# Performance work log

Measured on AMD Instinct MI355X. Metric: run time of the kernel, lower is better.

## Reference

```python
import jax, jax.numpy as jnp
import numpy as np

B, S, H = 1, 2048, 1024
E, F, K = 8, 3584, 2


def setup_inputs() -> dict:
    key = jax.random.key(0)
    ks = jax.random.split(key, 5)
    scale_h = 1.0 / np.sqrt(H)
    scale_f = 1.0 / np.sqrt(F)
    return {
        "hidden_states": jax.random.normal(ks[0], (B, S, H), dtype=jnp.float32),
        "gate_w": jax.random.normal(ks[1], (E, H), dtype=jnp.float32) * scale_h,
        "w1": jax.random.normal(ks[2], (E, F, H), dtype=jnp.float32) * scale_h,
        "w2": jax.random.normal(ks[3], (E, H, F), dtype=jnp.float32) * scale_f,
        "w3": jax.random.normal(ks[4], (E, F, H), dtype=jnp.float32) * scale_h,
    }


def reference(hidden_states, gate_w, w1, w2, w3):
    b, s, h = hidden_states.shape
    x = hidden_states.reshape(-1, h)                      # [T, H]
    T = x.shape[0]
    router_logits = x @ gate_w.T                          # [T, E]
    probs = jax.nn.softmax(router_logits.astype(jnp.float32), axis=-1)
    rw, sel = jax.lax.top_k(probs, K)                     # [T, K]
    rw = rw / jnp.sum(rw, axis=-1, keepdims=True)
    rw = rw.astype(x.dtype)
    # combine weights per (token, expert): scatter top-k routing weights
    combine = jnp.zeros((T, E), dtype=x.dtype).at[
        jnp.arange(T)[:, None], sel
    ].add(rw)                                             # [T, E]
    out = jnp.zeros_like(x)
    for e in range(E):  # small fixed expert count
        # SwiGLU expert FFN (F.linear: x @ W.T)
        hmid = jax.nn.silu(x @ w1[e].T) * (x @ w3[e].T)   # [T, F]
        out = out + combine[:, e:e + 1] * (hmid @ w2[e].T)
    return out.reshape(b, s, h), router_logits
```

## Files before the change

kernel.cpp:

```cpp
#include <hip/hip_runtime.h>
#include <hip/hip_bf16.h>
#include <math.h>

namespace {
constexpr int kT = 2048;
constexpr int kH = 1024;
constexpr int kE = 8;
constexpr int kF = 3584;
constexpr int kK = 2;

constexpr size_t OFF_CNT  = 0;
constexpr size_t OFF_LIST = 1024;
constexpr size_t OFF_RW   = OFF_LIST + sizeof(int) * kE * kT;
constexpr size_t OFF_HMID = 1u << 20;
constexpr size_t OFF_XB   = 32u << 20;
constexpr size_t SZ_XB    = (size_t)kT * kH * 2;
constexpr size_t SZ_W     = (size_t)kE * kF * kH * 2;
constexpr size_t OFF_W1B  = OFF_XB + SZ_XB;
constexpr size_t OFF_W3B  = OFF_W1B + SZ_W;
constexpr size_t OFF_W2B  = OFF_W3B + SZ_W;
constexpr size_t WS_NEED  = OFF_W2B + SZ_W;

constexpr long NX8  = (long)kT * kH / 8;
constexpr long NW8  = (long)kE * kF * kH / 8;
constexpr long TOT8 = NX8 + 3 * NW8;

typedef __attribute__((ext_vector_type(8))) short bf16x8;
typedef __attribute__((ext_vector_type(4))) float fx4;
}

__device__ __forceinline__ short f2bf_s(float f) {
  union { __hip_bfloat16 h; short s; } u;
  u.h = __float2bfloat16(f);
  return u.s;
}

__device__ __forceinline__ bf16x8 pack8(float4 a, float4 b) {
  bf16x8 r;
  r[0] = f2bf_s(a.x); r[1] = f2bf_s(a.y);
  r[2] = f2bf_s(a.z); r[3] = f2bf_s(a.w);
  r[4] = f2bf_s(b.x); r[5] = f2bf_s(b.y);
  r[6] = f2bf_s(b.z); r[7] = f2bf_s(b.w);
  return r;
}

__device__ __forceinline__ bf16x8 pack8v(fx4 a, fx4 b) {
  bf16x8 r;
  r[0] = f2bf_s(a[0]); r[1] = f2bf_s(a[1]);
  r[2] = f2bf_s(a[2]); r[3] = f2bf_s(a[3]);
  r[4] = f2bf_s(b[0]); r[5] = f2bf_s(b[1]);
  r[6] = f2bf_s(b[2]); r[7] = f2bf_s(b[3]);
  return r;
}

__device__ __forceinline__ int swz(int row, int u) {
  return row * 64 + ((u ^ (row & 7)) << 3);
}

__device__ __forceinline__ void gload16(const void* g, void* l) {
  __builtin_amdgcn_global_load_lds(
      (const __attribute__((address_space(1))) void*)g,
      (__attribute__((address_space(3))) void*)l, 16, 0, 0);
}

__global__ __launch_bounds__(256) void cast_all_kernel(
    const float* __restrict__ x, const float* __restrict__ w1,
    const float* __restrict__ w3, const float* __restrict__ w2,
    unsigned short* __restrict__ dst) {
  long i = (long)blockIdx.x * blockDim.x + threadIdx.x;
  const long stride = (long)gridDim.x * blockDim.x;
  for (; i < TOT8; i += stride) {
    const float* s; long o;
    if (i < NX8)              { s = x;  o = i; }
    else if (i < NX8 + NW8)   { s = w1; o = i - NX8; }
    else if (i < NX8 + 2*NW8) { s = w3; o = i - NX8 - NW8; }
    else                      { s = w2; o = i - NX8 - 2*NW8; }
    const fx4* sp = reinterpret_cast<const fx4*>(s + o * 8);
    const fx4 v0 = __builtin_nontemporal_load(sp);
    const fx4 v1 = __builtin_nontemporal_load(sp + 1);
    *reinterpret_cast<bf16x8*>(dst + i * 8) = pack8v(v0, v1);
  }
}

__global__ __launch_bounds__(256) void router_kernel(
    const float* __restrict__ x, const float* __restrict__ gw,
    float* __restrict__ logits_out, int* __restrict__ cnt,
    int* __restrict__ list, float* __restrict__ rw) {
  const int t = blockIdx.x;
  const float* xt = x + (size_t)t * kH;
  __shared__ float lg[kE];
  const int wave = threadIdx.x >> 6;
  const int lane = threadIdx.x & 63;
  for (int e = wave; e < kE; e += 4) {
    const float* g = gw + (size_t)e * kH;
    float s = 0.f;
    for (int h = lane; h < kH; h += 64) s += xt[h] * g[h];
#pragma unroll
    for (int off = 32; off > 0; off >>= 1) s += __shfl_down(s, off, 64);
    if (lane == 0) lg[e] = s;
  }
  __syncthreads();
  if (threadIdx.x < kE) logits_out[(size_t)t * kE + threadIdx.x] = lg[threadIdx.x];
  if (threadIdx.x == 0) {
    float m = lg[0];
#pragma unroll
    for (int e = 1; e < kE; ++e) m = fmaxf(m, lg[e]);
    float p[kE];
#pragma unroll
    for (int e = 0; e < kE; ++e) p[e] = expf(lg[e] - m);
    int i0 = 0;
#pragma unroll
    for (int e = 1; e < kE; ++e) if (p[e] > p[i0]) i0 = e;
    int i1 = (i0 == 0) ? 1 : 0;
#pragma unroll
    for (int e = 0; e < kE; ++e)
      if (e != i0 && e != i1 && p[e] > p[i1]) i1 = e;
    const float w0 = p[i0], w1v = p[i1];
    const float inv = 1.f / (w0 + w1v);
    rw[t * kK + 0] = w0 * inv;
    rw[t * kK + 1] = w1v * inv;
    const int s0 = atomicAdd(&cnt[i0], 1);
    list[i0 * kT + s0] = t * kK + 0;
    const int s1 = atomicAdd(&cnt[i1], 1);
    list[i1 * kT + s1] = t * kK + 1;
  }
}


__global__ __launch_bounds__(256) void moe_mid_gl(
    const unsigned short* __restrict__ xb, const unsigned short* __restrict__ w1b,
    const unsigned short* __restrict__ w3b, const int* __restrict__ cnt,
    const int* __restrict__ list, unsigned short* __restrict__ hmid) {
  const int e = blockIdx.z;
  const int n = cnt[e];
  const int t0 = blockIdx.y * 128;
  if (t0 >= n) return;
  const int f0 = blockIdx.x * 64;

  __shared__ short As[2][128 * 64];
  __shared__ short B1s[2][64 * 64];
  __shared__ short B3s[2][64 * 64];
  __shared__ int ppid[128];
  __shared__ int ptok[128];

  const int tid = threadIdx.x;
  if (tid < 128) {
    const int idx = t0 + tid;
    const int pid = (idx < n) ? list[e * kT + idx] : -1;
    ppid[tid] = pid;
    ptok[tid] = (pid < 0) ? 0 : (pid >> 1);
  }
  __syncthreads();

  const unsigned short* w1e = w1b + (size_t)e * kF * kH;
  const unsigned short* w3e = w3b + (size_t)e * kF * kH;

  const unsigned short* a_src[4];
#pragma unroll
  for (int c = 0; c < 4; ++c) {
    const int flat = tid + 256 * c;
    const int row = flat >> 3, u = flat & 7;
    a_src[c] = xb + (size_t)ptok[row] * kH + ((u ^ (row & 7)) * 8);
  }
  const unsigned short* b1_src[2]; const unsigned short* b3_src[2];
#pragma unroll
  for (int c = 0; c < 2; ++c) {
    const int flat = tid + 256 * c;
    const int row = flat >> 3, u = flat & 7;
    const int co = (u ^ (row & 7)) * 8;
    b1_src[c] = w1e + (size_t)(f0 + row) * kH + co;
    b3_src[c] = w3e + (size_t)(f0 + row) * kH + co;
  }

  const int lane = tid & 63, wid = tid >> 6;
  const int wr = wid >> 1, wc = wid & 1;
  const int lr = lane & 15, lq = lane >> 4;

  int aofs[2][4], bofs[2][2];
#pragma unroll
  for (int ks = 0; ks < 2; ++ks) {
#pragma unroll
    for (int mi = 0; mi < 4; ++mi)
      aofs[ks][mi] = swz(wr * 64 + mi * 16 + lr, ks * 4 + lq);
#pragma unroll
    for (int ni = 0; ni < 2; ++ni)
      bofs[ks][ni] = swz(wc * 32 + ni * 16 + lr, ks * 4 + lq);
  }

  fx4 acc1[4][2], acc3[4][2];
#pragma unroll
  for (int i = 0; i < 4; ++i)
#pragma unroll
    for (int j = 0; j < 2; ++j) { acc1[i][j] = (fx4)(0.f); acc3[i][j] = (fx4)(0.f); }

  auto STAGE = [&](int buf, int k0) {
#pragma unroll
    for (int c = 0; c < 4; ++c)
      gload16(a_src[c] + k0, &As[buf][(tid + 256 * c) * 8]);
#pragma unroll
    for (int c = 0; c < 2; ++c) {
      gload16(b1_src[c] + k0, &B1s[buf][(tid + 256 * c) * 8]);
      gload16(b3_src[c] + k0, &B3s[buf][(tid + 256 * c) * 8]);
    }
  };
  auto MFMA_PHASE = [&](int buf) {
    const short* Ab = As[buf]; const short* B1b = B1s[buf]; const short* B3b = B3s[buf];
    __builtin_amdgcn_s_setprio(1);
#pragma unroll
    for (int ks = 0; ks < 2; ++ks) {
      bf16x8 a[4], bb1[2], bb3[2];
#pragma unroll
      for (int mi = 0; mi < 4; ++mi)
        a[mi] = *reinterpret_cast<const bf16x8*>(&Ab[aofs[ks][mi]]);
#pragma unroll
      for (int ni = 0; ni < 2; ++ni) {
        bb1[ni] = *reinterpret_cast<const bf16x8*>(&B1b[bofs[ks][ni]]);
        bb3[ni] = *reinterpret_cast<const bf16x8*>(&B3b[bofs[ks][ni]]);
      }
#pragma unroll
      for (int mi = 0; mi < 4; ++mi)
#pragma unroll
        for (int ni = 0; ni < 2; ++ni) {
          acc1[mi][ni] = __builtin_amdgcn_mfma_f32_16x16x32_bf16(a[mi], bb1[ni], acc1[mi][ni], 0, 0, 0);
          acc3[mi][ni] = __builtin_amdgcn_mfma_f32_16x16x32_bf16(a[mi], bb3[ni], acc3[mi][ni], 0, 0, 0);
        }
    }
    __builtin_amdgcn_s_setprio(0);
  };

  constexpr int NIT = kH / 64;
  STAGE(0, 0);
  STAGE(1, 64);
  for (int it = 0; it < NIT; ++it) {
    const int cur = it & 1;
    if (it + 1 < NIT) asm volatile("s_waitcnt vmcnt(8)" ::: "memory");
    else              asm volatile("s_waitcnt vmcnt(0)" ::: "memory");
    asm volatile("s_barrier" ::: "memory");
    MFMA_PHASE(cur);
    asm volatile("s_barrier" ::: "memory");
    if (it + 2 < NIT) STAGE(cur, (it + 2) * 64);
  }

#pragma unroll
  for (int mi = 0; mi < 4; ++mi)
#pragma unroll
    for (int i = 0; i < 4; ++i) {
      const int row = wr * 64 + mi * 16 + lq * 4 + i;
      const int pid = ppid[row];
      if (pid < 0) continue;
#pragma unroll
      for (int ni = 0; ni < 2; ++ni) {
        const int col = f0 + wc * 32 + ni * 16 + lr;
        const float s1 = acc1[mi][ni][i];
        const float s3 = acc3[mi][ni][i];
        const float h = s1 * s3 / (1.f + expf(-s1));
        hmid[(size_t)pid * kF + col] = (unsigned short)f2bf_s(h);
      }
    }
}

__global__ __launch_bounds__(256) void moe_out_gl(
    const unsigned short* __restrict__ hmid, const unsigned short* __restrict__ w2b,
    const int* __restrict__ cnt, const int* __restrict__ list,
    const float* __restrict__ rw, float* __restrict__ out) {
  const int e = blockIdx.z;
  const int n = cnt[e];
  const int p0 = blockIdx.y * 128;
  if (p0 >= n) return;
  const int h0 = blockIdx.x * 64;

  __shared__ short As[2][128 * 64];
  __shared__ short Bs[2][64 * 64];
  __shared__ int ppid[128];
  __shared__ int prow[128];

  const int tid = threadIdx.x;
  if (tid < 128) {
    const int idx = p0 + tid;
    const int pid = (idx < n) ? list[e * kT + idx] : -1;
    ppid[tid] = pid;
    prow[tid] = (pid < 0) ? 0 : pid;
  }
  __syncthreads();

  const unsigned short* w2e = w2b + (size_t)e * kH * kF;

  const unsigned short* a_src[4];
#pragma unroll
  for (int c = 0; c < 4; ++c) {
    const int flat = tid + 256 * c;
    const int row = flat >> 3, u = flat & 7;
    a_src[c] = hmid + (size_t)prow[row] * kF + ((u ^ (row & 7)) * 8);
  }
  const unsigned short* b_src[2];
#pragma unroll
  for (int c = 0; c < 2; ++c) {
    const int flat = tid + 256 * c;
    const int row = flat >> 3, u = flat & 7;
    b_src[c] = w2e + (size_t)(h0 + row) * kF + ((u ^ (row & 7)) * 8);
  }

  const int lane = tid & 63, wid = tid >> 6;
  const int wr = wid >> 1, wc = wid & 1;
  const int lr = lane & 15, lq = lane >> 4;

  int aofs[2][4], bofs[2][2];
#pragma unroll
  for (int ks = 0; ks < 2; ++ks) {
#pragma unroll
    for (int mi = 0; mi < 4; ++mi)
      aofs[ks][mi] = swz(wr * 64 + mi * 16 + lr, ks * 4 + lq);
#pragma unroll
    for (int ni = 0; ni < 2; ++ni)
      bofs[ks][ni] = swz(wc * 32 + ni * 16 + lr, ks * 4 + lq);
  }

  fx4 acc[4][2];
#pragma unroll
  for (int i = 0; i < 4; ++i)
#pragma unroll
    for (int j = 0; j < 2; ++j) acc[i][j] = (fx4)(0.f);

  auto STAGE = [&](int buf, int k0) {
#pragma unroll
    for (int c = 0; c < 4; ++c)
      gload16(a_src[c] + k0, &As[buf][(tid + 256 * c) * 8]);
#pragma unroll
    for (int c = 0; c < 2; ++c)
      gload16(b_src[c] + k0, &Bs[buf][(tid + 256 * c) * 8]);
  };
  auto MFMA_PHASE = [&](int buf) {
    const short* Ab = As[buf]; const short* Bb = Bs[buf];
    __builtin_amdgcn_s_setprio(1);
#pragma unroll
    for (int ks = 0; ks < 2; ++ks) {
      bf16x8 a[4], b[2];
#pragma unroll
      for (int mi = 0; mi < 4; ++mi)
        a[mi] = *reinterpret_cast<const bf16x8*>(&Ab[aofs[ks][mi]]);
#pragma unroll
      for (int ni = 0; ni < 2; ++ni)
        b[ni] = *reinterpret_cast<const bf16x8*>(&Bb[bofs[ks][ni]]);
#pragma unroll
      for (int mi = 0; mi < 4; ++mi)
#pragma unroll
        for (int ni = 0; ni < 2; ++ni)
          acc[mi][ni] = __builtin_amdgcn_mfma_f32_16x16x32_bf16(a[mi], b[ni], acc[mi][ni], 0, 0, 0);
    }
    __builtin_amdgcn_s_setprio(0);
  };

  constexpr int NIT = kF / 64;
  STAGE(0, 0);
  STAGE(1, 64);
  for (int it = 0; it < NIT; ++it) {
    const int cur = it & 1;
    if (it + 1 < NIT) asm volatile("s_waitcnt vmcnt(6)" ::: "memory");
    else              asm volatile("s_waitcnt vmcnt(0)" ::: "memory");
    asm volatile("s_barrier" ::: "memory");
    MFMA_PHASE(cur);
    asm volatile("s_barrier" ::: "memory");
    if (it + 2 < NIT) STAGE(cur, (it + 2) * 64);
  }

#pragma unroll
  for (int mi = 0; mi < 4; ++mi)
#pragma unroll
    for (int i = 0; i < 4; ++i) {
      const int row = wr * 64 + mi * 16 + lq * 4 + i;
      const int pid = ppid[row];
      if (pid < 0) continue;
      const int tok = pid >> 1;
      const float w = rw[pid];
      float* op = out + (size_t)tok * kH + h0 + wc * 32 + lr;
#pragma unroll
      for (int ni = 0; ni < 2; ++ni)
        atomicAdd(&op[ni * 16], w * acc[mi][ni][i]);
    }
}

struct StageM { float4 a[2][2], b1[2][2], b3[2][2]; };

__global__ __launch_bounds__(256) void moe_mid_mfma(
    const float* __restrict__ x, const float* __restrict__ w1,
    const float* __restrict__ w3, const int* __restrict__ cnt,
    const int* __restrict__ list, unsigned short* __restrict__ hmid) {
  const int e = blockIdx.z;
  const int n = cnt[e];
  const int t0 = blockIdx.y * 64;
  if (t0 >= n) return;
  const int f0 = blockIdx.x * 64;

  __shared__ short As[2][64 * 64];
  __shared__ short B1s[2][64 * 64];
  __shared__ short B3s[2][64 * 64];
  __shared__ int ppid[64];
  __shared__ int ptok[64];

  const int tid = threadIdx.x;
  if (tid < 64) {
    const int idx = t0 + tid;
    const int pid = (idx < n) ? list[e * kT + idx] : -1;
    ppid[tid] = pid;
    ptok[tid] = (pid < 0) ? 0 : (pid >> 1);
  }
  __syncthreads();

  const float* w1e = w1 + (size_t)e * kF * kH;
  const float* w3e = w3 + (size_t)e * kF * kH;

  const float* a_src[2]; const float* b1_src[2]; const float* b3_src[2];
  int sw_[2];
#pragma unroll
  for (int i = 0; i < 2; ++i) {
    const int flat = tid + 256 * i;
    const int row = flat >> 3, u = flat & 7;
    a_src[i]  = x + (size_t)ptok[row] * kH + u * 8;
    b1_src[i] = w1e + (size_t)(f0 + row) * kH + u * 8;
    b3_src[i] = w3e + (size_t)(f0 + row) * kH + u * 8;
    sw_[i] = swz(row, u);
  }

  const int lane = tid & 63, wid = tid >> 6;
  const int wr = wid >> 1, wc = wid & 1;
  const int lr = lane & 15, lq = lane >> 4;

  fx4 acc1[2][2], acc3[2][2];
#pragma unroll
  for (int i = 0; i < 2; ++i)
#pragma unroll
    for (int j = 0; j < 2; ++j) { acc1[i][j] = (fx4)(0.f); acc3[i][j] = (fx4)(0.f); }

  auto LOAD = [&](StageM& S, int k0) {
#pragma unroll
    for (int i = 0; i < 2; ++i) {
      S.a[i][0]  = *reinterpret_cast<const float4*>(a_src[i] + k0);
      S.a[i][1]  = *reinterpret_cast<const float4*>(a_src[i] + k0 + 4);
      S.b1[i][0] = *reinterpret_cast<const float4*>(b1_src[i] + k0);
      S.b1[i][1] = *reinterpret_cast<const float4*>(b1_src[i] + k0 + 4);
      S.b3[i][0] = *reinterpret_cast<const float4*>(b3_src[i] + k0);
      S.b3[i][1] = *reinterpret_cast<const float4*>(b3_src[i] + k0 + 4);
    }
  };
  auto STORE = [&](const StageM& S, int buf) {
#pragma unroll
    for (int i = 0; i < 2; ++i) {
      *reinterpret_cast<bf16x8*>(&As[buf][sw_[i]])  = pack8(S.a[i][0], S.a[i][1]);
      *reinterpret_cast<bf16x8*>(&B1s[buf][sw_[i]]) = pack8(S.b1[i][0], S.b1[i][1]);
      *reinterpret_cast<bf16x8*>(&B3s[buf][sw_[i]]) = pack8(S.b3[i][0], S.b3[i][1]);
    }
  };
  auto MFMA_PHASE = [&](int buf) {
    const short* Ab = As[buf]; const short* B1b = B1s[buf]; const short* B3b = B3s[buf];
    __builtin_amdgcn_s_setprio(1);
#pragma unroll
    for (int ks = 0; ks < 2; ++ks) {
      bf16x8 a[2], bb1[2], bb3[2];
#pragma unroll
      for (int mi = 0; mi < 2; ++mi)
        a[mi] = *reinterpret_cast<const bf16x8*>(&Ab[swz(wr * 32 + mi * 16 + lr, ks * 4 + lq)]);
#pragma unroll
      for (int ni = 0; ni < 2; ++ni) {
        bb1[ni] = *reinterpret_cast<const bf16x8*>(&B1b[swz(wc * 32 + ni * 16 + lr, ks * 4 + lq)]);
        bb3[ni] = *reinterpret_cast<const bf16x8*>(&B3b[swz(wc * 32 + ni * 16 + lr, ks * 4 + lq)]);
      }
#pragma unroll
      for (int mi = 0; mi < 2; ++mi)
#pragma unroll
        for (int ni = 0; ni < 2; ++ni) {
          acc1[mi][ni] = __builtin_amdgcn_mfma_f32_16x16x32_bf16(a[mi], bb1[ni], acc1[mi][ni], 0, 0, 0);
          acc3[mi][ni] = __builtin_amdgcn_mfma_f32_16x16x32_bf16(a[mi], bb3[ni], acc3[mi][ni], 0, 0, 0);
        }
    }
    __builtin_amdgcn_s_setprio(0);
  };

  StageM R0, R1;
  constexpr int NIT = kH / 64;
  LOAD(R0, 0);
  LOAD(R1, 64);
  STORE(R0, 0);
  __syncthreads();
#pragma unroll 2
  for (int it = 0; it < NIT; ++it) {
    if (it & 1) {
      if (it + 2 < NIT) LOAD(R1, (it + 2) * 64);
      MFMA_PHASE(1);
      if (it + 1 < NIT) STORE(R0, 0);
    } else {
      if (it + 2 < NIT) LOAD(R0, (it + 2) * 64);
      MFMA_PHASE(0);
      if (it + 1 < NIT) STORE(R1, 1);
    }
    __syncthreads();
  }

#pragma unroll
  for (int mi = 0; mi < 2; ++mi)
#pragma unroll
    for (int i = 0; i < 4; ++i) {
      const int row = wr * 32 + mi * 16 + lq * 4 + i;
      const int pid = ppid[row];
      if (pid < 0) continue;
#pragma unroll
      for (int ni = 0; ni < 2; ++ni) {
        const int col = f0 + wc * 32 + ni * 16 + lr;
        const float s1 = acc1[mi][ni][i];
        const float s3 = acc3[mi][ni][i];
        const float h = s1 * s3 / (1.f + expf(-s1));
        hmid[(size_t)pid * kF + col] = (unsigned short)f2bf_s(h);
      }
    }
}

struct StageO { bf16x8 a[2]; float4 b[2][2]; };

__global__ __launch_bounds__(256) void moe_out_mfma(
    const unsigned short* __restrict__ hmid, const float* __restrict__ w2,
    const int* __restrict__ cnt, const int* __restrict__ list,
    const float* __restrict__ rw, float* __restrict__ out) {
  const int e = blockIdx.z;
  const int n = cnt[e];
  const int p0 = blockIdx.y * 64;
  if (p0 >= n) return;
  const int h0 = blockIdx.x * 64;

  __shared__ short As[2][64 * 64];
  __shared__ short Bs[2][64 * 64];
  __shared__ int ppid[64];
  __shared__ int prow[64];

  const int tid = threadIdx.x;
  if (tid < 64) {
    const int idx = p0 + tid;
    const int pid = (idx < n) ? list[e * kT + idx] : -1;
    ppid[tid] = pid;
    prow[tid] = (pid < 0) ? 0 : pid;
  }
  __syncthreads();

  const float* w2e = w2 + (size_t)e * kH * kF;

  const unsigned short* a_src[2]; const float* b_src[2];
  int sw_[2];
#pragma unroll
  for (int i = 0; i < 2; ++i) {
    const int flat = tid + 256 * i;
    const int row = flat >> 3, u = flat & 7;
    a_src[i] = hmid + (size_t)prow[row] * kF + u * 8;
    b_src[i] = w2e + (size_t)(h0 + row) * kF + u * 8;
    sw_[i] = swz(row, u);
  }

  const int lane = tid & 63, wid = tid >> 6;
  const int wr = wid >> 1, wc = wid & 1;
  const int lr = lane & 15, lq = lane >> 4;

  fx4 acc[2][2];
#pragma unroll
  for (int i = 0; i < 2; ++i)
#pragma unroll
    for (int j = 0; j < 2; ++j) acc[i][j] = (fx4)(0.f);

  auto LOAD = [&](StageO& S, int k0) {
#pragma unroll
    for (int i = 0; i < 2; ++i) {
      S.a[i]    = *reinterpret_cast<const bf16x8*>(a_src[i] + k0);
      S.b[i][0] = *reinterpret_cast<const float4*>(b_src[i] + k0);
      S.b[i][1] = *reinterpret_cast<const float4*>(b_src[i] + k0 + 4);
    }
  };
  auto STORE = [&](const StageO& S, int buf) {
#pragma unroll
    for (int i = 0; i < 2; ++i) {
      *reinterpret_cast<bf16x8*>(&As[buf][sw_[i]]) = S.a[i];
      *reinterpret_cast<bf16x8*>(&Bs[buf][sw_[i]]) = pack8(S.b[i][0], S.b[i][1]);
    }
  };
  auto MFMA_PHASE = [&](int buf) {
    const short* Ab = As[buf]; const short* Bb = Bs[buf];
    __builtin_amdgcn_s_setprio(1);
#pragma unroll
    for (int ks = 0; ks < 2; ++ks) {
      bf16x8 a[2], b[2];
#pragma unroll
      for (int mi = 0; mi < 2; ++mi)
        a[mi] = *reinterpret_cast<const bf16x8*>(&Ab[swz(wr * 32 + mi * 16 + lr, ks * 4 + lq)]);
#pragma unroll
      for (int ni = 0; ni < 2; ++ni)
        b[ni] = *reinterpret_cast<const bf16x8*>(&Bb[swz(wc * 32 + ni * 16 + lr, ks * 4 + lq)]);
#pragma unroll
      for (int mi = 0; mi < 2; ++mi)
#pragma unroll
        for (int ni = 0; ni < 2; ++ni)
          acc[mi][ni] = __builtin_amdgcn_mfma_f32_16x16x32_bf16(a[mi], b[ni], acc[mi][ni], 0, 0, 0);
    }
    __builtin_amdgcn_s_setprio(0);
  };

  StageO R0, R1;
  constexpr int NIT = kF / 64;
  LOAD(R0, 0);
  LOAD(R1, 64);
  STORE(R0, 0);
  __syncthreads();
#pragma unroll 2
  for (int it = 0; it < NIT; ++it) {
    if (it & 1) {
      if (it + 2 < NIT) LOAD(R1, (it + 2) * 64);
      MFMA_PHASE(1);
      if (it + 1 < NIT) STORE(R0, 0);
    } else {
      if (it + 2 < NIT) LOAD(R0, (it + 2) * 64);
      MFMA_PHASE(0);
      if (it + 1 < NIT) STORE(R1, 1);
    }
    __syncthreads();
  }

#pragma unroll
  for (int mi = 0; mi < 2; ++mi)
#pragma unroll
    for (int i = 0; i < 4; ++i) {
      const int row = wr * 32 + mi * 16 + lq * 4 + i;
      const int pid = ppid[row];
      if (pid < 0) continue;
      const int tok = pid >> 1;
      const float w = rw[pid];
      float* op = out + (size_t)tok * kH + h0 + wc * 32 + lr;
#pragma unroll
      for (int ni = 0; ni < 2; ++ni)
        atomicAdd(&op[ni * 16], w * acc[mi][ni][i]);
    }
}

extern "C" void kernel_launch(void* const* d_in, const int* in_sizes, int n_in,
                              void* d_out, int out_size, void* d_ws,
                              size_t ws_size, hipStream_t stream) {
  (void)in_sizes; (void)n_in; (void)out_size;
  const float* x  = (const float*)d_in[0];
  const float* gw = (const float*)d_in[1];
  const float* w1 = (const float*)d_in[2];
  const float* w2 = (const float*)d_in[3];
  const float* w3 = (const float*)d_in[4];

  float* out    = (float*)d_out;
  float* logits = out + (size_t)kT * kH;

  char* ws = (char*)d_ws;
  int*            cnt  = (int*)(ws + OFF_CNT);
  int*            list = (int*)(ws + OFF_LIST);
  float*          rw   = (float*)(ws + OFF_RW);
  unsigned short* hmid = (unsigned short*)(ws + OFF_HMID);

  hipMemsetAsync(out, 0, (size_t)kT * kH * sizeof(float), stream);
  hipMemsetAsync(cnt, 0, kE * sizeof(int), stream);

  router_kernel<<<kT, 256, 0, stream>>>(x, gw, logits, cnt, list, rw);

  if (ws_size >= WS_NEED) {
    unsigned short* xb  = (unsigned short*)(ws + OFF_XB);
    unsigned short* w1b = (unsigned short*)(ws + OFF_W1B);
    unsigned short* w3b = (unsigned short*)(ws + OFF_W3B);
    unsigned short* w2b = (unsigned short*)(ws + OFF_W2B);

    cast_all_kernel<<<2048, 256, 0, stream>>>(x, w1, w3, w2, xb);

    dim3 g1(kF / 64, kT / 128, kE);
    moe_mid_gl<<<g1, 256, 0, stream>>>(xb, w1b, w3b, cnt, list, hmid);

    dim3 g2(kH / 64, kT / 128, kE);
    moe_out_gl<<<g2, 256, 0, stream>>>(hmid, w2b, cnt, list, rw, out);
  } else {
    dim3 g1(kF / 64, kT / 64, kE);
    moe_mid_mfma<<<g1, 256, 0, stream>>>(x, w1, w3, cnt, list, hmid);

    dim3 g2(kH / 64, kT / 64, kE);
    moe_out_mfma<<<g2, 256, 0, stream>>>(hmid, w2, cnt, list, rw, out);
  }
}
```

Before: 316.0 us.

## Switch moe_mid_gl to triple-buffered K=32 tiles with deeper prefetch

The gate/up GEMM kernel now stages K tiles of 32 instead of 64 and uses three LDS buffers instead of two. Two tiles are kept in flight while one is computed, and the swizzle is redone for 32-wide rows. LDS use drops from 64KB to 48KB, which may allow more blocks per CU. The cost is twice as many barriers and loop iterations, with less MFMA work between each sync.

```diff
diff --git a/kernel.cpp b/kernel.cpp
--- a/kernel.cpp
+++ b/kernel.cpp
@@ -55,6 +55,10 @@
 
 __device__ __forceinline__ int swz(int row, int u) {
   return row * 64 + ((u ^ (row & 7)) << 3);
+}
+
+__device__ __forceinline__ int swz32(int row, int u) {
+  return row * 32 + ((u ^ ((row >> 1) & 3)) << 3);
 }
 
 __device__ __forceinline__ void gload16(const void* g, void* l) {
@@ -137,9 +141,9 @@
   if (t0 >= n) return;
   const int f0 = blockIdx.x * 64;
 
-  __shared__ short As[2][128 * 64];
-  __shared__ short B1s[2][64 * 64];
-  __shared__ short B3s[2][64 * 64];
+  __shared__ short As[3][128 * 32];
+  __shared__ short B1s[3][64 * 32];
+  __shared__ short B3s[3][64 * 32];
   __shared__ int ppid[128];
   __shared__ int ptok[128];
 
@@ -155,37 +159,33 @@
   const unsigned short* w1e = w1b + (size_t)e * kF * kH;
   const unsigned short* w3e = w3b + (size_t)e * kF * kH;
 
-  const unsigned short* a_src[4];
-#pragma unroll
-  for (int c = 0; c < 4; ++c) {
-    const int flat = tid + 256 * c;
-    const int row = flat >> 3, u = flat & 7;
-    a_src[c] = xb + (size_t)ptok[row] * kH + ((u ^ (row & 7)) * 8);
-  }
-  const unsigned short* b1_src[2]; const unsigned short* b3_src[2];
+  const unsigned short* a_src[2];
 #pragma unroll
   for (int c = 0; c < 2; ++c) {
     const int flat = tid + 256 * c;
-    const int row = flat >> 3, u = flat & 7;
-    const int co = (u ^ (row & 7)) * 8;
-    b1_src[c] = w1e + (size_t)(f0 + row) * kH + co;
-    b3_src[c] = w3e + (size_t)(f0 + row) * kH + co;
+    const int row = flat >> 2, u = flat & 3;
+    a_src[c] = xb + (size_t)ptok[row] * kH + ((u ^ ((row >> 1) & 3)) * 8);
+  }
+  const unsigned short* b1_src;
+  const unsigned short* b3_src;
+  {
+    const int row = tid >> 2, u = tid & 3;
+    const int co = (u ^ ((row >> 1) & 3)) * 8;
+    b1_src = w1e + (size_t)(f0 + row) * kH + co;
+    b3_src = w3e + (size_t)(f0 + row) * kH + co;
   }
 
   const int lane = tid & 63, wid = tid >> 6;
   const int wr = wid >> 1, wc = wid & 1;
   const int lr = lane & 15, lq = lane >> 4;
 
-  int aofs[2][4], bofs[2][2];
-#pragma unroll
-  for (int ks = 0; ks < 2; ++ks) {
-#pragma unroll
-    for (int mi = 0; mi < 4; ++mi)
-      aofs[ks][mi] = swz(wr * 64 + mi * 16 + lr, ks * 4 + lq);
-#pragma unroll
-    for (int ni = 0; ni < 2; ++ni)
-      bofs[ks][ni] = swz(wc * 32 + ni * 16 + lr, ks * 4 + lq);
-  }
+  int aofs[4], bofs[2];
+#pragma unroll
+  for (int mi = 0; mi < 4; ++mi)
+    aofs[mi] = swz32(wr * 64 + mi * 16 + lr, lq);
+#pragma unroll
+  for (int ni = 0; ni < 2; ++ni)
+    bofs[ni] = swz32(wc * 32 + ni * 16 + lr, lq);
 
   fx4 acc1[4][2], acc3[4][2];
 #pragma unroll
@@ -195,50 +195,47 @@
 
   auto STAGE = [&](int buf, int k0) {
 #pragma unroll
-    for (int c = 0; c < 4; ++c)
+    for (int c = 0; c < 2; ++c)
       gload16(a_src[c] + k0, &As[buf][(tid + 256 * c) * 8]);
-#pragma unroll
-    for (int c = 0; c < 2; ++c) {
-      gload16(b1_src[c] + k0, &B1s[buf][(tid + 256 * c) * 8]);
-      gload16(b3_src[c] + k0, &B3s[buf][(tid + 256 * c) * 8]);
-    }
+    gload16(b1_src + k0, &B1s[buf][tid * 8]);
+    gload16(b3_src + k0, &B3s[buf][tid * 8]);
   };
   auto MFMA_PHASE = [&](int buf) {
     const short* Ab = As[buf]; const short* B1b = B1s[buf]; const short* B3b = B3s[buf];
     __builtin_amdgcn_s_setprio(1);
-#pragma unroll
-    for (int ks = 0; ks < 2; ++ks) {
-      bf16x8 a[4], bb1[2], bb3[2];
-#pragma unroll
-      for (int mi = 0; mi < 4; ++mi)
-        a[mi] = *reinterpret_cast<const bf16x8*>(&Ab[aofs[ks][mi]]);
+    bf16x8 a[4], bb1[2], bb3[2];
+#pragma unroll
+    for (int mi = 0; mi < 4; ++mi)
+      a[mi] = *reinterpret_cast<const bf16x8*>(&Ab[aofs[mi]]);
+#pragma unroll
+    for (int ni = 0; ni < 2; ++ni) {
+      bb1[ni] = *reinterpret_cast<const bf16x8*>(&B1b[bofs[ni]]);
+      bb3[ni] = *reinterpret_cast<const bf16x8*>(&B3b[bofs[ni]]);
+    }
+#pragma unroll
+    for (int mi = 0; mi < 4; ++mi)
 #pragma unroll
       for (int ni = 0; ni < 2; ++ni) {
-        bb1[ni] = *reinterpret_cast<const bf16x8*>(&B1b[bofs[ks][ni]]);
-        bb3[ni] = *reinterpret_cast<const bf16x8*>(&B3b[bofs[ks][ni]]);
+        acc1[mi][ni] = __builtin_amdgcn_mfma_f32_16x16x32_bf16(a[mi], bb1[ni], acc1[mi][ni], 0, 0, 0);
+        acc3[mi][ni] = __builtin_amdgcn_mfma_f32_16x16x32_bf16(a[mi], bb3[ni], acc3[mi][ni], 0, 0, 0);
       }
-#pragma unroll
-      for (int mi = 0; mi < 4; ++mi)
-#pragma unroll
-        for (int ni = 0; ni < 2; ++ni) {
-          acc1[mi][ni] = __builtin_amdgcn_mfma_f32_16x16x32_bf16(a[mi], bb1[ni], acc1[mi][ni], 0, 0, 0);
-          acc3[mi][ni] = __builtin_amdgcn_mfma_f32_16x16x32_bf16(a[mi], bb3[ni], acc3[mi][ni], 0, 0, 0);
-        }
-    }
     __builtin_amdgcn_s_setprio(0);
   };
 
-  constexpr int NIT = kH / 64;
+  constexpr int NIT = kH / 32;
   STAGE(0, 0);
-  STAGE(1, 64);
+  STAGE(1, 32);
+  STAGE(2, 64);
+  int buf = 0;
   for (int it = 0; it < NIT; ++it) {
-    const int cur = it & 1;
-    if (it + 1 < NIT) asm volatile("s_waitcnt vmcnt(8)" ::: "memory");
-    else              asm volatile("s_waitcnt vmcnt(0)" ::: "memory");
+    if (it < NIT - 2)       asm volatile("s_waitcnt vmcnt(8)" ::: "memory");
+    else if (it == NIT - 2) asm volatile("s_waitcnt vmcnt(4)" ::: "memory");
+    else                    asm volatile("s_waitcnt vmcnt(0)" ::: "memory");
     asm volatile("s_barrier" ::: "memory");
-    MFMA_PHASE(cur);
+    MFMA_PHASE(buf);
     asm volatile("s_barrier" ::: "memory");
-    if (it + 2 < NIT) STAGE(cur, (it + 2) * 64);
+    if (it + 3 < NIT) STAGE(buf, (it + 3) * 32);
+    buf = (buf == 2) ? 0 : buf + 1;
   }
 
 #pragma unroll
```

Result: no change. 312.8 us (median of 3 runs) (-1.0%).
